# Kernel optimization log

Measured on AMD Instinct MI355X. Metric: run time of the kernel, lower is better.

The kernel has to match this reference:

```python
import math
import jax, jax.numpy as jnp
import numpy as np

N, D, E, H = 4096, 512, 64, 8
LN_EPS = 1e-5


def setup_inputs() -> dict:
    key = jax.random.key(0)
    ks = jax.random.split(key, 6)
    return {
        "x": jax.random.normal(ks[0], (N, D), jnp.float32),
        "wq": jax.random.normal(ks[1], (H, D, E), jnp.float32) * 0.05,
        "wk": jax.random.normal(ks[2], (H, D, E), jnp.float32) * 0.05,
        "wv": jax.random.normal(ks[3], (H, D, E), jnp.float32) * 0.05,
        "w_mh": jax.random.normal(ks[4], (H * E, D), jnp.float32) * 0.05,
        "ln1_g": jnp.ones((D,), jnp.float32),
        "ln1_b": jnp.zeros((D,), jnp.float32),
        "ffn_w": jax.random.normal(ks[5], (D, D), jnp.float32) * 0.05,  # torch Linear weight [out,in]
        "ffn_b": jnp.zeros((D,), jnp.float32),
        "ln2_g": jnp.ones((D,), jnp.float32),
        "ln2_b": jnp.zeros((D,), jnp.float32),
    }


def _layernorm(y, g, b):
    m = y.mean(-1, keepdims=True)
    v = ((y - m) ** 2).mean(-1, keepdims=True)
    return (y - m) * jax.lax.rsqrt(v + LN_EPS) * g + b


def reference(x, wq, wk, wv, w_mh, ln1_g, ln1_b, ffn_w, ffn_b, ln2_g, ln2_b):
    dk = math.sqrt(wk.shape[-1])  # sqrt(embedding_size), as in the torch code
    q = jnp.einsum('nd,hde->hne', x, wq)  # [H,N,E]
    k = jnp.einsum('nd,hde->hne', x, wk)
    v = jnp.einsum('nd,hde->hne', x, wv)
    scores = jax.nn.softmax(jnp.einsum('hne,hme->hnm', q, k) / dk, axis=-1)  # [H,N,N]
    z = jnp.einsum('hnm,hme->hne', scores, v)  # [H,N,E]
    concat_z = jnp.transpose(z, (1, 0, 2)).reshape(x.shape[0], -1)  # [N, H*E]
    transformed_z = concat_z @ w_mh  # [N, D]
    normed_z = _layernorm(transformed_z + x, ln1_g, ln1_b)
    out = normed_z @ ffn_w.T + ffn_b  # nn.Linear
    return _layernorm(out + normed_z, ln2_g, ln2_b)
```

## Files before the change

kernel.cpp:

```cpp
#include <hip/hip_runtime.h>

#define NN 4096
#define DD 512
#define EE 64
#define HH 8

typedef _Float16 f16;
typedef f16 f16x2 __attribute__((ext_vector_type(2)));
typedef f16 f16x4 __attribute__((ext_vector_type(4)));
typedef f16 f16x8 __attribute__((ext_vector_type(8)));
typedef float f32x4 __attribute__((ext_vector_type(4)));
typedef __fp16 fp16x2 __attribute__((ext_vector_type(2)));

__device__ __forceinline__ float hexp2(float x) { return __builtin_amdgcn_exp2f(x); }
__device__ __forceinline__ f16x2 pkrtz(float a, float b) {
    fp16x2 r = __builtin_amdgcn_cvt_pkrtz(a, b);
    return __builtin_bit_cast(f16x2, r);
}
union f16x4u { f16x4 v4; f16x2 v2[2]; };
union f16x8u { f16x8 v8; f16x2 v2[4]; };
union f32x8u { float a[8]; f32x4 v[2]; };

__device__ void tile_transpose_cvt(const float* __restrict__ src, f16* __restrict__ dst,
                                   int R, int C, int bx, int by, int tid)
{
    __shared__ float t[32][33];
    const int tx = tid & 31, ty = tid >> 5;
    #pragma unroll
    for (int i = 0; i < 4; ++i) {
        int r = ty + i * 8;
        t[r][tx] = src[(size_t)(by + r) * C + bx + tx];
    }
    __syncthreads();
    #pragma unroll
    for (int i = 0; i < 4; ++i) {
        int c = ty + i * 8;
        dst[(size_t)(bx + c) * R + by + tx] = (f16)t[tx][c];
    }
}

__global__ __launch_bounds__(256) void prep_kernel(
    const float* __restrict__ x, const float* __restrict__ ffn_w,
    const float* __restrict__ wq, const float* __restrict__ wk, const float* __restrict__ wv,
    const float* __restrict__ w_mh,
    f16* __restrict__ xh, f16* __restrict__ ffnT, f16* __restrict__ wqkvT, f16* __restrict__ wmhT)
{
    const int job = blockIdx.y;
    const int tid = threadIdx.x;
    if (job == 0) {
        size_t i = ((size_t)blockIdx.x * 256 + tid) * 4;
        const size_t step = (size_t)256 * 256 * 4;
        for (; i < (size_t)NN * DD; i += step) {
            float4 t = *(const float4*)(x + i);
            f16x4 h = { (f16)t.x, (f16)t.y, (f16)t.z, (f16)t.w };
            *(f16x4*)(xh + i) = h;
        }
    } else if (job == 1) {
        size_t i = ((size_t)blockIdx.x * 256 + tid) * 4;
        float4 t = *(const float4*)(ffn_w + i);
        f16x4 h = { (f16)t.x, (f16)t.y, (f16)t.z, (f16)t.w };
        *(f16x4*)(ffnT + i) = h;
    } else if (job <= 4) {
        const float* src = (job == 2) ? wq : (job == 3) ? wk : wv;
        f16* dst = wqkvT + (size_t)(job - 2) * HH * EE * DD;
        const int z = blockIdx.x >> 5;
        const int tile = blockIdx.x & 31;
        tile_transpose_cvt(src + (size_t)z * DD * EE, dst + (size_t)z * DD * EE,
                           DD, EE, (tile & 1) * 32, (tile >> 1) * 32, tid);
    } else {
        const int tile = blockIdx.x;
        tile_transpose_cvt(w_mh, wmhT, DD, DD, (tile & 15) * 32, (tile >> 4) * 32, tid);
    }
}

__global__ __launch_bounds__(256) void qkv_mfma_kernel(
    const f16* __restrict__ A, const f16* __restrict__ BT,
    f16* __restrict__ qh, f16* __restrict__ kh, f16* __restrict__ vTh)
{
    __shared__ f16 As[2][64][72];
    __shared__ f16 Bs[2][64][72];
    const int tid = threadIdx.x;
    const int n0 = blockIdx.x * 64;
    const int cb = blockIdx.y;
    const int sel = cb >> 3, h = cb & 7;
    const f16* Arow = A + (size_t)n0 * DD;
    const f16* Brow = BT + (size_t)cb * 64 * DD;

    const int lane = tid & 63, wave = tid >> 6;
    const int l16 = lane & 15, quad = lane >> 4;
    const int m0 = wave * 16;

    const int r1 = tid >> 3, c1 = (tid & 7) * 8;
    const int r2 = (tid + 256) >> 3, c2 = ((tid + 256) & 7) * 8;

    f32x4 acc[4];
    #pragma unroll
    for (int t = 0; t < 4; ++t) acc[t] = (f32x4){0.f, 0.f, 0.f, 0.f};

    f16x8 a1 = *(const f16x8*)(Arow + (size_t)r1 * DD + c1);
    f16x8 a2 = *(const f16x8*)(Arow + (size_t)r2 * DD + c2);
    f16x8 b1 = *(const f16x8*)(Brow + (size_t)r1 * DD + c1);
    f16x8 b2 = *(const f16x8*)(Brow + (size_t)r2 * DD + c2);

    int buf = 0;
    for (int kt = 0; kt < DD; kt += 64) {
        *(f16x8*)(&As[buf][r1][c1]) = a1;
        *(f16x8*)(&As[buf][r2][c2]) = a2;
        *(f16x8*)(&Bs[buf][r1][c1]) = b1;
        *(f16x8*)(&Bs[buf][r2][c2]) = b2;
        __syncthreads();
        if (kt + 64 < DD) {
            a1 = *(const f16x8*)(Arow + (size_t)r1 * DD + kt + 64 + c1);
            a2 = *(const f16x8*)(Arow + (size_t)r2 * DD + kt + 64 + c2);
            b1 = *(const f16x8*)(Brow + (size_t)r1 * DD + kt + 64 + c1);
            b2 = *(const f16x8*)(Brow + (size_t)r2 * DD + kt + 64 + c2);
        }
        #pragma unroll
        for (int kk = 0; kk < 64; kk += 32) {
            f16x8 a = *(const f16x8*)(&As[buf][m0 + l16][kk + quad * 8]);
            #pragma unroll
            for (int t = 0; t < 4; ++t) {
                f16x8 b = *(const f16x8*)(&Bs[buf][t * 16 + l16][kk + quad * 8]);
                acc[t] = __builtin_amdgcn_mfma_f32_16x16x32_f16(a, b, acc[t], 0, 0, 0);
            }
        }
        buf ^= 1;
    }

    if (sel == 2) {
        #pragma unroll
        for (int t = 0; t < 4; ++t) {
            int e = t * 16 + l16;
            f16x4 v = { (f16)acc[t][0], (f16)acc[t][1], (f16)acc[t][2], (f16)acc[t][3] };
            *(f16x4*)(vTh + ((size_t)h * EE + e) * NN + n0 + m0 + quad * 4) = v;
        }
    } else {
        f16* o = (sel == 0) ? qh : kh;
        const float s = (sel == 0) ? 0.125f * 1.44269504088896f : 1.0f;
        #pragma unroll
        for (int r = 0; r < 4; ++r) {
            int row = n0 + m0 + quad * 4 + r;
            #pragma unroll
            for (int t = 0; t < 4; ++t)
                o[(size_t)h * NN * EE + (size_t)row * EE + t * 16 + l16] = (f16)(acc[t][r] * s);
        }
    }
}

#define BQ 256
#define NSTRIP 4
#define BK 64
#define LK (BK + 12)

__global__ __launch_bounds__(256) void attn_mfma_kernel(
    const f16* __restrict__ q, const f16* __restrict__ k,
    const f16* __restrict__ vT, f16* __restrict__ Opart, float* __restrict__ lpart)
{
    __shared__ f16 Ks[BK][LK];
    __shared__ f16 VsT[EE][LK];

    const int tid = threadIdx.x;
    const int h = blockIdx.x;
    const int n0 = blockIdx.y * BQ;
    const int sp = blockIdx.z;
    const int nsp = gridDim.z;
    const int wave = tid >> 6;
    const int lane = tid & 63;
    const int l16 = lane & 15;
    const int quad = lane >> 4;
    const int m0 = wave * 16;

    const f16* qh = q + (size_t)h * NN * EE;
    const f16* kh = k + (size_t)h * NN * EE;
    const f16* vh = vT + (size_t)h * NN * EE;

    f16x8 qf[NSTRIP][2];
    #pragma unroll
    for (int s = 0; s < NSTRIP; ++s) {
        const f16* qb = qh + (size_t)(n0 + s * 64 + m0 + l16) * EE;
        qf[s][0] = *(const f16x8*)(qb + quad * 8);
        qf[s][1] = *(const f16x8*)(qb + 32 + quad * 8);
    }

    float lp[NSTRIP];
    f32x4 O[NSTRIP][4];
    #pragma unroll
    for (int s = 0; s < NSTRIP; ++s) {
        lp[s] = 0.f;
        #pragma unroll
        for (int t = 0; t < 4; ++t) O[s][t] = (f32x4){0.f, 0.f, 0.f, 0.f};
    }

    const int span = NN / nsp;
    const int k_begin = sp * span;
    const int k_end = k_begin + span;

    const int srow = tid >> 3, sc8 = (tid & 7) * 8;
    const int srow2 = (tid + 256) >> 3, sc82 = ((tid + 256) & 7) * 8;
    #define KPERM(kk_) (((kk_) & 0x23) | (((kk_) & 0x04) << 2) | (((kk_) & 0x18) >> 1))
    const int prow1 = KPERM(srow), prow2 = KPERM(srow2);

    f16x8 kr0 = *(const f16x8*)(kh + (size_t)(k_begin + srow) * EE + sc8);
    f16x8 kr1 = *(const f16x8*)(kh + (size_t)(k_begin + srow2) * EE + sc82);
    f16x8 vr0 = *(const f16x8*)(vh + (size_t)srow * NN + k_begin + sc8);
    f16x8 vr1 = *(const f16x8*)(vh + (size_t)srow2 * NN + k_begin + sc82);

    for (int kt = k_begin; kt < k_end; kt += BK) {
        __syncthreads();
        *(f16x8*)(&Ks[prow1][sc8]) = kr0;
        *(f16x8*)(&Ks[prow2][sc82]) = kr1;
        *(f16x8*)(&VsT[srow][sc8]) = vr0;
        *(f16x8*)(&VsT[srow2][sc82]) = vr1;
        __syncthreads();

        if (kt + BK < k_end) {
            kr0 = *(const f16x8*)(kh + (size_t)(kt + BK + srow) * EE + sc8);
            kr1 = *(const f16x8*)(kh + (size_t)(kt + BK + srow2) * EE + sc82);
            vr0 = *(const f16x8*)(vh + (size_t)srow * NN + kt + BK + sc8);
            vr1 = *(const f16x8*)(vh + (size_t)srow2 * NN + kt + BK + sc82);
        }

        f16x8 bf[NSTRIP][2];
        #pragma unroll
        for (int t = 0; t < 4; ++t) {
            f16x8 a0 = *(const f16x8*)(&Ks[t * 16 + l16][quad * 8]);
            f16x8 a1 = *(const f16x8*)(&Ks[t * 16 + l16][32 + quad * 8]);
            #pragma unroll
            for (int s = 0; s < NSTRIP; ++s) {
                f32x4 st = {0.f, 0.f, 0.f, 0.f};
                st = __builtin_amdgcn_mfma_f32_16x16x32_f16(a0, qf[s][0], st, 0, 0, 0);
                st = __builtin_amdgcn_mfma_f32_16x16x32_f16(a1, qf[s][1], st, 0, 0, 0);
                float p0 = hexp2(st[0]);
                float p1 = hexp2(st[1]);
                float p2 = hexp2(st[2]);
                float p3 = hexp2(st[3]);
                lp[s] += (p0 + p1) + (p2 + p3);
                f16x2* bp = (f16x2*)&bf[s][t >> 1];
                const int o2 = (t & 1) * 2;
                bp[o2 + 0] = pkrtz(p0, p1);
                bp[o2 + 1] = pkrtz(p2, p3);
            }
        }

        #pragma unroll
        for (int te = 0; te < 4; ++te) {
            f16x8 v0 = *(const f16x8*)(&VsT[te * 16 + l16][quad * 8]);
            f16x8 v1 = *(const f16x8*)(&VsT[te * 16 + l16][32 + quad * 8]);
            #pragma unroll
            for (int s = 0; s < NSTRIP; ++s) {
                O[s][te] = __builtin_amdgcn_mfma_f32_16x16x32_f16(v0, bf[s][0], O[s][te], 0, 0, 0);
                O[s][te] = __builtin_amdgcn_mfma_f32_16x16x32_f16(v1, bf[s][1], O[s][te], 0, 0, 0);
            }
        }
    }

    #pragma unroll
    for (int s = 0; s < NSTRIP; ++s) {
        float l = lp[s];
        l += __shfl_xor(l, 16);
        l += __shfl_xor(l, 32);
        const int row = n0 + s * 64 + m0 + l16;
        if (quad == 0)
            lpart[(size_t)sp * HH * NN + (size_t)h * NN + row] = l;
        const float inv = 1.f / l;
        f16* obase = Opart + ((size_t)sp * NN + row) * DD + h * EE;
        #pragma unroll
        for (int te = 0; te < 4; ++te) {
            f16x4u v;
            v.v2[0] = pkrtz(O[s][te][0] * inv, O[s][te][1] * inv);
            v.v2[1] = pkrtz(O[s][te][2] * inv, O[s][te][3] * inv);
            *(f16x4*)(obase + te * 16 + quad * 4) = v.v4;
        }
    }
}

template<int NSP>
__global__ __launch_bounds__(256) void gemmz_mfma_kernel(
    const f16* __restrict__ Opart, const float* __restrict__ lpart,
    const f16* __restrict__ BT, const f16* __restrict__ resid16,
    f16* __restrict__ out, float* __restrict__ pstat)
{
    __shared__ f16 As[2][64][72];
    __shared__ f16 Bs[2][64][72];
    const int tid = threadIdx.x;
    const int n0 = blockIdx.x * 64;
    const int jb = blockIdx.y;
    const int j0 = jb * 64;
    const f16* Brow = BT + (size_t)j0 * DD;

    const int lane = tid & 63, wave = tid >> 6;
    const int l16 = lane & 15, quad = lane >> 4;
    const int m0 = wave * 16;

    const int r1 = tid >> 3, c1 = (tid & 7) * 8;
    const int r2 = (tid + 256) >> 3, c2 = ((tid + 256) & 7) * 8;

    f32x4 acc[4];
    #pragma unroll
    for (int t = 0; t < 4; ++t) acc[t] = (f32x4){0.f, 0.f, 0.f, 0.f};

    f16x8 op1[NSP], op2[NSP];
    #pragma unroll
    for (int s = 0; s < NSP; ++s) {
        op1[s] = *(const f16x8*)(Opart + ((size_t)s * NN + n0 + r1) * DD + c1);
        op2[s] = *(const f16x8*)(Opart + ((size_t)s * NN + n0 + r2) * DD + c2);
    }
    f16x8 b1 = *(const f16x8*)(Brow + (size_t)r1 * DD + c1);
    f16x8 b2 = *(const f16x8*)(Brow + (size_t)r2 * DD + c2);

    int buf = 0;
    for (int kt = 0; kt < DD; kt += 64) {
        const int h = kt >> 6;
        float lw1[NSP], lw2[NSP], s1 = 0.f, s2 = 0.f;
        #pragma unroll
        for (int s = 0; s < NSP; ++s) {
            lw1[s] = lpart[(size_t)s * HH * NN + (size_t)h * NN + n0 + r1];
            lw2[s] = lpart[(size_t)s * HH * NN + (size_t)h * NN + n0 + r2];
            s1 += lw1[s]; s2 += lw2[s];
        }
        const float i1 = 1.f / s1, i2 = 1.f / s2;
        float aw1[8], aw2[8];
        #pragma unroll
        for (int i = 0; i < 8; ++i) { aw1[i] = 0.f; aw2[i] = 0.f; }
        #pragma unroll
        for (int s = 0; s < NSP; ++s) {
            const float w1 = lw1[s] * i1, w2 = lw2[s] * i2;
            #pragma unroll
            for (int i = 0; i < 8; ++i) {
                aw1[i] += w1 * (float)op1[s][i];
                aw2[i] += w2 * (float)op2[s][i];
            }
        }
        f16x8u av1, av2;
        #pragma unroll
        for (int i = 0; i < 4; ++i) {
            av1.v2[i] = pkrtz(aw1[2 * i], aw1[2 * i + 1]);
            av2.v2[i] = pkrtz(aw2[2 * i], aw2[2 * i + 1]);
        }
        *(f16x8*)(&As[buf][r1][c1]) = av1.v8;
        *(f16x8*)(&As[buf][r2][c2]) = av2.v8;
        *(f16x8*)(&Bs[buf][r1][c1]) = b1;
        *(f16x8*)(&Bs[buf][r2][c2]) = b2;
        __syncthreads();
        if (kt + 64 < DD) {
            #pragma unroll
            for (int s = 0; s < NSP; ++s) {
                op1[s] = *(const f16x8*)(Opart + ((size_t)s * NN + n0 + r1) * DD + kt + 64 + c1);
                op2[s] = *(const f16x8*)(Opart + ((size_t)s * NN + n0 + r2) * DD + kt + 64 + c2);
            }
            b1 = *(const f16x8*)(Brow + (size_t)r1 * DD + kt + 64 + c1);
            b2 = *(const f16x8*)(Brow + (size_t)r2 * DD + kt + 64 + c2);
        }
        #pragma unroll
        for (int kk = 0; kk < 64; kk += 32) {
            f16x8 a = *(const f16x8*)(&As[buf][m0 + l16][kk + quad * 8]);
            #pragma unroll
            for (int t = 0; t < 4; ++t) {
                f16x8 b = *(const f16x8*)(&Bs[buf][t * 16 + l16][kk + quad * 8]);
                acc[t] = __builtin_amdgcn_mfma_f32_16x16x32_f16(a, b, acc[t], 0, 0, 0);
            }
        }
        buf ^= 1;
    }

    float vv[4][4];
    #pragma unroll
    for (int r = 0; r < 4; ++r) {
        int row = n0 + m0 + quad * 4 + r;
        #pragma unroll
        for (int t = 0; t < 4; ++t) {
            int col = j0 + t * 16 + l16;
            float v = acc[t][r] + (float)resid16[(size_t)row * DD + col];
            vv[r][t] = v;
            out[(size_t)row * DD + col] = (f16)v;
        }
    }
    #pragma unroll
    for (int r = 0; r < 4; ++r) {
        float s = (vv[r][0] + vv[r][1]) + (vv[r][2] + vv[r][3]);
        float q = (vv[r][0] * vv[r][0] + vv[r][1] * vv[r][1])
                + (vv[r][2] * vv[r][2] + vv[r][3] * vv[r][3]);
        s += __shfl_xor(s, 1); q += __shfl_xor(q, 1);
        s += __shfl_xor(s, 2); q += __shfl_xor(q, 2);
        s += __shfl_xor(s, 4); q += __shfl_xor(q, 4);
        s += __shfl_xor(s, 8); q += __shfl_xor(q, 8);
        if (l16 == 0) {
            int row = n0 + m0 + quad * 4 + r;
            pstat[(size_t)jb * NN + row] = s;
            pstat[(size_t)(8 + jb) * NN + row] = q;
        }
    }
}

__global__ __launch_bounds__(256) void gemmln2_kernel(
    const f16* __restrict__ y16, const float* __restrict__ pstat,
    const f16* __restrict__ BT, const float* __restrict__ bias,
    const float* __restrict__ lng, const float* __restrict__ lnb,
    f16* __restrict__ out)
{
    __shared__ f16 As[2][64][72];
    __shared__ f16 Bs[2][64][72];
    const int tid = threadIdx.x;
    const int n0 = blockIdx.x * 64;
    const int j0 = blockIdx.y * 64;
    const f16* Brow = BT + (size_t)j0 * DD;

    const int lane = tid & 63, wave = tid >> 6;
    const int l16 = lane & 15, quad = lane >> 4;
    const int m0 = wave * 16;

    const int r1 = tid >> 3, c1 = (tid & 7) * 8;
    const int r2 = (tid + 256) >> 3, c2 = ((tid + 256) & 7) * 8;

    float s1 = 0.f, q1 = 0.f, s2 = 0.f, q2 = 0.f;
    #pragma unroll
    for (int jb = 0; jb < 8; ++jb) {
        s1 += pstat[(size_t)jb * NN + n0 + r1];
        q1 += pstat[(size_t)(8 + jb) * NN + n0 + r1];
        s2 += pstat[(size_t)jb * NN + n0 + r2];
        q2 += pstat[(size_t)(8 + jb) * NN + n0 + r2];
    }
    const float m1 = s1 * (1.f / DD), m2 = s2 * (1.f / DD);
    const float iv1 = rsqrtf(q1 * (1.f / DD) - m1 * m1 + 1e-5f);
    const float iv2 = rsqrtf(q2 * (1.f / DD) - m2 * m2 + 1e-5f);

    f32x4 acc[4];
    #pragma unroll
    for (int t = 0; t < 4; ++t) acc[t] = (f32x4){0.f, 0.f, 0.f, 0.f};

    f16x8 a1 = *(const f16x8*)(y16 + (size_t)(n0 + r1) * DD + c1);
    f16x8 a2 = *(const f16x8*)(y16 + (size_t)(n0 + r2) * DD + c2);
    f16x8 b1 = *(const f16x8*)(Brow + (size_t)r1 * DD + c1);
    f16x8 b2 = *(const f16x8*)(Brow + (size_t)r2 * DD + c2);

    int buf = 0;
    for (int kt = 0; kt < DD; kt += 64) {
        f32x8u gu, bu;
        gu.v[0] = *(const f32x4*)(lng + kt + c1);
        gu.v[1] = *(const f32x4*)(lng + kt + c1 + 4);
        bu.v[0] = *(const f32x4*)(lnb + kt + c1);
        bu.v[1] = *(const f32x4*)(lnb + kt + c1 + 4);
        f16x8u av1, av2;
        #pragma unroll
        for (int i = 0; i < 4; ++i) {
            float x0 = ((float)a1[2 * i]     - m1) * iv1 * gu.a[2 * i]     + bu.a[2 * i];
            float x1 = ((float)a1[2 * i + 1] - m1) * iv1 * gu.a[2 * i + 1] + bu.a[2 * i + 1];
            float y0 = ((float)a2[2 * i]     - m2) * iv2 * gu.a[2 * i]     + bu.a[2 * i];
            float y1 = ((float)a2[2 * i + 1] - m2) * iv2 * gu.a[2 * i + 1] + bu.a[2 * i + 1];
            av1.v2[i] = pkrtz(x0, x1);
            av2.v2[i] = pkrtz(y0, y1);
        }
        *(f16x8*)(&As[buf][r1][c1]) = av1.v8;
        *(f16x8*)(&As[buf][r2][c2]) = av2.v8;
        *(f16x8*)(&Bs[buf][r1][c1]) = b1;
        *(f16x8*)(&Bs[buf][r2][c2]) = b2;
        __syncthreads();
        if (kt + 64 < DD) {
            a1 = *(const f16x8*)(y16 + (size_t)(n0 + r1) * DD + kt + 64 + c1);
            a2 = *(const f16x8*)(y16 + (size_t)(n0 + r2) * DD + kt + 64 + c2);
            b1 = *(const f16x8*)(Brow + (size_t)r1 * DD + kt + 64 + c1);
            b2 = *(const f16x8*)(Brow + (size_t)r2 * DD + kt + 64 + c2);
        }
        #pragma unroll
        for (int kk = 0; kk < 64; kk += 32) {
            f16x8 a = *(const f16x8*)(&As[buf][m0 + l16][kk + quad * 8]);
            #pragma unroll
            for (int t = 0; t < 4; ++t) {
                f16x8 b = *(const f16x8*)(&Bs[buf][t * 16 + l16][kk + quad * 8]);
                acc[t] = __builtin_amdgcn_mfma_f32_16x16x32_f16(a, b, acc[t], 0, 0, 0);
            }
        }
        buf ^= 1;
    }

    #pragma unroll
    for (int r = 0; r < 4; ++r) {
        const int row = n0 + m0 + quad * 4 + r;
        float ss = 0.f, qq = 0.f;
        #pragma unroll
        for (int jb = 0; jb < 8; ++jb) {
            ss += pstat[(size_t)jb * NN + row];
            qq += pstat[(size_t)(8 + jb) * NN + row];
        }
        const float mr = ss * (1.f / DD);
        const float ir = rsqrtf(qq * (1.f / DD) - mr * mr + 1e-5f);
        #pragma unroll
        for (int t = 0; t < 4; ++t) {
            const int col = j0 + t * 16 + l16;
            float nz = ((float)y16[(size_t)row * DD + col] - mr) * ir * lng[col] + lnb[col];
            float v = acc[t][r] + bias[col] + nz;
            out[(size_t)row * DD + col] = (f16)v;
        }
    }
}

__global__ __launch_bounds__(256) void ln_kernel(
    const f16* __restrict__ y, const float* __restrict__ g, const float* __restrict__ b,
    float* __restrict__ of)
{
    const int lane = threadIdx.x & 63, wave = threadIdx.x >> 6;
    const int row = blockIdx.x * 4 + wave;
    f16x8 v = *(const f16x8*)(y + (size_t)row * DD + lane * 8);
    float vf[8];
    float s = 0.f, q = 0.f;
    #pragma unroll
    for (int i = 0; i < 8; ++i) {
        vf[i] = (float)v[i];
        s += vf[i];
        q += vf[i] * vf[i];
    }
    #pragma unroll
    for (int o = 1; o < 64; o <<= 1) { s += __shfl_xor(s, o); q += __shfl_xor(q, o); }
    float mean = s * (1.f / DD);
    float var = q * (1.f / DD) - mean * mean;
    float inv = rsqrtf(var + 1e-5f);

    f32x4 g0 = *(const f32x4*)(g + lane * 8);
    f32x4 g1 = *(const f32x4*)(g + lane * 8 + 4);
    f32x4 b0 = *(const f32x4*)(b + lane * 8);
    f32x4 b1 = *(const f32x4*)(b + lane * 8 + 4);
    f32x4 f0, f1;
    #pragma unroll
    for (int i = 0; i < 4; ++i) {
        f0[i] = (vf[i] - mean) * inv * g0[i] + b0[i];
        f1[i] = (vf[i + 4] - mean) * inv * g1[i] + b1[i];
    }
    *(f32x4*)(of + (size_t)row * DD + lane * 8) = f0;
    *(f32x4*)(of + (size_t)row * DD + lane * 8 + 4) = f1;
}

extern "C" void kernel_launch(void* const* d_in, const int* in_sizes, int n_in,
                              void* d_out, int out_size, void* d_ws, size_t ws_size,
                              hipStream_t stream) {
    const float* x     = (const float*)d_in[0];
    const float* wq    = (const float*)d_in[1];
    const float* wk    = (const float*)d_in[2];
    const float* wv    = (const float*)d_in[3];
    const float* w_mh  = (const float*)d_in[4];
    const float* ln1_g = (const float*)d_in[5];
    const float* ln1_b = (const float*)d_in[6];
    const float* ffn_w = (const float*)d_in[7];
    const float* ffn_b = (const float*)d_in[8];
    const float* ln2_g = (const float*)d_in[9];
    const float* ln2_b = (const float*)d_in[10];
    float* out = (float*)d_out;

    const size_t poolBytes = ((size_t)3 * HH * EE * DD + 2 * (size_t)DD * DD
                            + 3 * (size_t)HH * NN * EE + 3 * (size_t)NN * DD) * 2
                            + (size_t)16 * NN * 4;
    int SP = 2;
    {
        size_t need4 = (size_t)4 * NN * DD * 2 + (size_t)4 * HH * NN * 4 + poolBytes + 4096;
        if (ws_size >= need4) SP = 4;
    }

    char* base = (char*)d_ws;
    f16* Opart = (f16*)base;
    float* lpart = (float*)(base + (size_t)SP * NN * DD * 2);
    size_t regionA = (size_t)SP * NN * DD * 2 + (size_t)SP * HH * NN * 4;
    regionA = (regionA + 255) & ~(size_t)255;
    f16* p = (f16*)(base + regionA);
    f16* wqkvT  = p; p += (size_t)3 * HH * EE * DD;
    f16* wmhT   = p; p += (size_t)DD * DD;
    f16* ffnT   = p; p += (size_t)DD * DD;
    f16* qh     = p; p += (size_t)HH * NN * EE;
    f16* kh     = p; p += (size_t)HH * NN * EE;
    f16* vTh    = p; p += (size_t)HH * NN * EE;
    f16* y16    = p; p += (size_t)NN * DD;
    f16* y2     = p; p += (size_t)NN * DD;
    f16* xh     = p; p += (size_t)NN * DD;
    float* pstat = (float*)p;

    prep_kernel<<<dim3(256, 6), 256, 0, stream>>>(x, ffn_w, wq, wk, wv, w_mh,
                                                  xh, ffnT, wqkvT, wmhT);

    qkv_mfma_kernel<<<dim3(NN / 64, 24), 256, 0, stream>>>(xh, wqkvT, qh, kh, vTh);
    attn_mfma_kernel<<<dim3(HH, NN / BQ, SP), 256, 0, stream>>>(qh, kh, vTh, Opart, lpart);
    if (SP == 4)
        gemmz_mfma_kernel<4><<<dim3(NN / 64, DD / 64), 256, 0, stream>>>(Opart, lpart, wmhT, xh, y16, pstat);
    else
        gemmz_mfma_kernel<2><<<dim3(NN / 64, DD / 64), 256, 0, stream>>>(Opart, lpart, wmhT, xh, y16, pstat);
    gemmln2_kernel<<<dim3(NN / 64, DD / 64), 256, 0, stream>>>(y16, pstat, ffnT, ffn_b, ln1_g, ln1_b, y2);
    ln_kernel<<<dim3(NN / 4), 256, 0, stream>>>(y2, ln2_g, ln2_b, out);
}
```

Baseline: 180.2 us.

## Enlarge QKV GEMM row tile to 128 and halve attention query block

The QKV projection kernel now computes 128 rows per block, with each wave doing two 16-row MFMA strips that share the same B fragments. Its LDS is single-buffered with two barriers per k-step instead of a double buffer, and the V store uses packed round-toward-zero conversion. The attention kernel's query block shrinks from 256 to 128 with two strips, which doubles the grid for better occupancy. The trade-offs are fewer QKV blocks, an extra barrier per k-step, and more K/V reloads in attention.

```diff
diff --git a/kernel.cpp b/kernel.cpp
--- a/kernel.cpp
+++ b/kernel.cpp
@@ -77,10 +77,10 @@
     const f16* __restrict__ A, const f16* __restrict__ BT,
     f16* __restrict__ qh, f16* __restrict__ kh, f16* __restrict__ vTh)
 {
-    __shared__ f16 As[2][64][72];
-    __shared__ f16 Bs[2][64][72];
+    __shared__ f16 As[128][72];
+    __shared__ f16 Bs[64][72];
     const int tid = threadIdx.x;
-    const int n0 = blockIdx.x * 64;
+    const int n0 = blockIdx.x * 128;
     const int cb = blockIdx.y;
     const int sel = cb >> 3, h = cb & 7;
     const f16* Arow = A + (size_t)n0 * DD;
@@ -88,67 +88,94 @@
 
     const int lane = tid & 63, wave = tid >> 6;
     const int l16 = lane & 15, quad = lane >> 4;
-    const int m0 = wave * 16;
-
-    const int r1 = tid >> 3, c1 = (tid & 7) * 8;
-    const int r2 = (tid + 256) >> 3, c2 = ((tid + 256) & 7) * 8;
-
-    f32x4 acc[4];
-    #pragma unroll
-    for (int t = 0; t < 4; ++t) acc[t] = (f32x4){0.f, 0.f, 0.f, 0.f};
-
-    f16x8 a1 = *(const f16x8*)(Arow + (size_t)r1 * DD + c1);
-    f16x8 a2 = *(const f16x8*)(Arow + (size_t)r2 * DD + c2);
-    f16x8 b1 = *(const f16x8*)(Brow + (size_t)r1 * DD + c1);
-    f16x8 b2 = *(const f16x8*)(Brow + (size_t)r2 * DD + c2);
-
-    int buf = 0;
+    const int m0 = wave * 32;
+
+    f32x4 acc[2][4];
+    #pragma unroll
+    for (int i = 0; i < 2; ++i)
+        #pragma unroll
+        for (int t = 0; t < 4; ++t) acc[i][t] = (f32x4){0.f, 0.f, 0.f, 0.f};
+
+    f16x8 ar[4], br[2];
+    #pragma unroll
+    for (int i = 0; i < 4; ++i) {
+        int c = tid + i * 256;
+        ar[i] = *(const f16x8*)(Arow + (size_t)(c >> 3) * DD + (c & 7) * 8);
+    }
+    #pragma unroll
+    for (int i = 0; i < 2; ++i) {
+        int c = tid + i * 256;
+        br[i] = *(const f16x8*)(Brow + (size_t)(c >> 3) * DD + (c & 7) * 8);
+    }
+
     for (int kt = 0; kt < DD; kt += 64) {
-        *(f16x8*)(&As[buf][r1][c1]) = a1;
-        *(f16x8*)(&As[buf][r2][c2]) = a2;
-        *(f16x8*)(&Bs[buf][r1][c1]) = b1;
-        *(f16x8*)(&Bs[buf][r2][c2]) = b2;
         __syncthreads();
+        #pragma unroll
+        for (int i = 0; i < 4; ++i) {
+            int c = tid + i * 256;
+            *(f16x8*)(&As[c >> 3][(c & 7) * 8]) = ar[i];
+        }
+        #pragma unroll
+        for (int i = 0; i < 2; ++i) {
+            int c = tid + i * 256;
+            *(f16x8*)(&Bs[c >> 3][(c & 7) * 8]) = br[i];
+        }
+        __syncthreads();
+
         if (kt + 64 < DD) {
-            a1 = *(const f16x8*)(Arow + (size_t)r1 * DD + kt + 64 + c1);
-            a2 = *(const f16x8*)(Arow + (size_t)r2 * DD + kt + 64 + c2);
-            b1 = *(const f16x8*)(Brow + (size_t)r1 * DD + kt + 64 + c1);
-            b2 = *(const f16x8*)(Brow + (size_t)r2 * DD + kt + 64 + c2);
-        }
+            #pragma unroll
+            for (int i = 0; i < 4; ++i) {
+                int c = tid + i * 256;
+                ar[i] = *(const f16x8*)(Arow + (size_t)(c >> 3) * DD + kt + 64 + (c & 7) * 8);
+            }
+            #pragma unroll
+            for (int i = 0; i < 2; ++i) {
+                int c = tid + i * 256;
+                br[i] = *(const f16x8*)(Brow + (size_t)(c >> 3) * DD + kt + 64 + (c & 7) * 8);
+            }
+        }
+
         #pragma unroll
         for (int kk = 0; kk < 64; kk += 32) {
-            f16x8 a = *(const f16x8*)(&As[buf][m0 + l16][kk + quad * 8]);
+            f16x8 af0 = *(const f16x8*)(&As[m0 + l16][kk + quad * 8]);
+            f16x8 af1 = *(const f16x8*)(&As[m0 + 16 + l16][kk + quad * 8]);
             #pragma unroll
             for (int t = 0; t < 4; ++t) {
-                f16x8 b = *(const f16x8*)(&Bs[buf][t * 16 + l16][kk + quad * 8]);
-                acc[t] = __builtin_amdgcn_mfma_f32_16x16x32_f16(a, b, acc[t], 0, 0, 0);
-            }
-        }
-        buf ^= 1;
+                f16x8 b = *(const f16x8*)(&Bs[t * 16 + l16][kk + quad * 8]);
+                acc[0][t] = __builtin_amdgcn_mfma_f32_16x16x32_f16(af0, b, acc[0][t], 0, 0, 0);
+                acc[1][t] = __builtin_amdgcn_mfma_f32_16x16x32_f16(af1, b, acc[1][t], 0, 0, 0);
+            }
+        }
     }
 
     if (sel == 2) {
         #pragma unroll
-        for (int t = 0; t < 4; ++t) {
-            int e = t * 16 + l16;
-            f16x4 v = { (f16)acc[t][0], (f16)acc[t][1], (f16)acc[t][2], (f16)acc[t][3] };
-            *(f16x4*)(vTh + ((size_t)h * EE + e) * NN + n0 + m0 + quad * 4) = v;
-        }
+        for (int i = 0; i < 2; ++i)
+            #pragma unroll
+            for (int t = 0; t < 4; ++t) {
+                int e = t * 16 + l16;
+                f16x4u v;
+                v.v2[0] = pkrtz(acc[i][t][0], acc[i][t][1]);
+                v.v2[1] = pkrtz(acc[i][t][2], acc[i][t][3]);
+                *(f16x4*)(vTh + ((size_t)h * EE + e) * NN + n0 + m0 + i * 16 + quad * 4) = v.v4;
+            }
     } else {
         f16* o = (sel == 0) ? qh : kh;
         const float s = (sel == 0) ? 0.125f * 1.44269504088896f : 1.0f;
         #pragma unroll
-        for (int r = 0; r < 4; ++r) {
-            int row = n0 + m0 + quad * 4 + r;
-            #pragma unroll
-            for (int t = 0; t < 4; ++t)
-                o[(size_t)h * NN * EE + (size_t)row * EE + t * 16 + l16] = (f16)(acc[t][r] * s);
-        }
-    }
-}
-
-#define BQ 256
-#define NSTRIP 4
+        for (int i = 0; i < 2; ++i)
+            #pragma unroll
+            for (int r = 0; r < 4; ++r) {
+                int row = n0 + m0 + i * 16 + quad * 4 + r;
+                #pragma unroll
+                for (int t = 0; t < 4; ++t)
+                    o[(size_t)h * NN * EE + (size_t)row * EE + t * 16 + l16] = (f16)(acc[i][t][r] * s);
+            }
+    }
+}
+
+#define BQ 128
+#define NSTRIP 2
 #define BK 64
 #define LK (BK + 12)
 
@@ -574,7 +601,7 @@
     prep_kernel<<<dim3(256, 6), 256, 0, stream>>>(x, ffn_w, wq, wk, wv, w_mh,
                                                   xh, ffnT, wqkvT, wmhT);
 
-    qkv_mfma_kernel<<<dim3(NN / 64, 24), 256, 0, stream>>>(xh, wqkvT, qh, kh, vTh);
+    qkv_mfma_kernel<<<dim3(NN / 128, 24), 256, 0, stream>>>(xh, wqkvT, qh, kh, vTh);
     attn_mfma_kernel<<<dim3(HH, NN / BQ, SP), 256, 0, stream>>>(qh, kh, vTh, Opart, lpart);
     if (SP == 4)
         gemmz_mfma_kernel<4><<<dim3(NN / 64, DD / 64), 256, 0, stream>>>(Opart, lpart, wmhT, xh, y16, pstat);
```

Measured after the change: 176.8 us. Within noise of the previous version (-1.9%).
